# Performance work log

Hardware: AMD Instinct MI355X
Metric: run time of the kernel (lower is better)

Reference implementation:

```python
import jax, jax.numpy as jnp
import numpy as np

V, D, B, NEG = 100000, 128, 4096, 5
D_INNER = int(D * 2.0 * 2 / 3)  # nGPT FF inner dim = 170

def l2norm(t, axis=-1):
    return t / jnp.linalg.norm(t, axis=axis, keepdims=True)

def setup_inputs() -> dict:
    key = jax.random.key(0)
    ks = jax.random.split(key, 8)
    return {
        "input_ids": jax.random.randint(ks[0], (B,), 0, V),
        "target_ids": jax.random.randint(ks[1], (B,), 0, V),
        "neg_ids": jax.random.randint(ks[2], (B, NEG), 0, V),
        "W_in": jax.random.normal(ks[3], (V, D), jnp.float32) * (1.0 / np.sqrt(D)),
        "W_out": jax.random.normal(ks[4], (V, D), jnp.float32) * (1.0 / np.sqrt(D)),
        "W_hidden": jax.random.normal(ks[5], (D_INNER, D), jnp.float32) * 0.02,
        "W_gate": jax.random.normal(ks[6], (D_INNER, D), jnp.float32) * 0.02,
        "W_ff_out": jax.random.normal(ks[7], (D, D_INNER), jnp.float32) * 0.02,
        "hidden_scale": jnp.ones((D_INNER,), jnp.float32),
        "gate_scale": jnp.ones((D_INNER,), jnp.float32),
        "logit_scale": jnp.full((V,), D ** -0.5, dtype=jnp.float32),  # Scale param init = s_logit_scale
    }

def reference(input_ids, target_ids, neg_ids, W_in, W_out, W_hidden, W_gate,
              W_ff_out, hidden_scale, gate_scale, logit_scale):
    # skipgram: gather normalized input embeddings
    emb = l2norm(W_in)[input_ids]                                  # (B, D)
    # nGPT FeedForward: silu-gated, weights l2-normalized on input dim
    h = (emb @ l2norm(W_hidden).T) * hidden_scale                  # (B, D_INNER)
    g = (emb @ l2norm(W_gate).T) * gate_scale * jnp.sqrt(jnp.float32(D))
    x = jax.nn.silu(g) * h
    x = x @ l2norm(W_ff_out, axis=0).T                             # (B, D), to_out norm_dim_in=False
    # logits over full vocab, scaled by Scale(): param * (init/scale)
    scale_eff = logit_scale * (1.0 / (D ** -0.5))                  # (V,)
    logits = (x @ l2norm(W_out).T) * scale_eff                     # (B, V)
    # negative-sampling loss: gather positive + sampled negative logits
    pos = jnp.take_along_axis(logits, target_ids[:, None], axis=1)  # (B, 1)
    neg = jnp.take_along_axis(logits, neg_ids, axis=1)              # (B, NEG)
    positive_loss = jax.nn.log_sigmoid(pos).mean()
    negative_loss = jax.nn.log_sigmoid(-neg).mean()
    return -(positive_loss + negative_loss)
```

## Files before the change

kernel.cpp:

```cpp
#include <hip/hip_runtime.h>
#include <math.h>

#define DD    128
#define DI    170
#define DIP   176
#define ND4   32
#define ND4H  16
#define NI4P  44
#define BB    4096
#define NNEG  5
#define ROWS  8
#define NBLK  (BB / ROWS)
#define NTHR  512
#define NTASK (ROWS * (1 + NNEG))
#define XOP   132
#define SQRT_D 11.3137084989847603904f

#define WS_WHT 0
#define WS_WGT (ND4 * DIP * 4)
#define WS_WFT (2 * ND4 * DIP * 4)

__device__ __forceinline__ float wave_bcast_sum(float v) {
#pragma unroll
    for (int m = 1; m < 64; m <<= 1) v += __shfl_xor(v, m, 64);
    return v;
}

__global__ __launch_bounds__(256) void prep_kernel(
    const float* __restrict__ W_hidden,
    const float* __restrict__ W_gate,
    const float* __restrict__ W_ff_out,
    const float* __restrict__ hidden_scale,
    const float* __restrict__ gate_scale,
    float* __restrict__ ws,
    float* __restrict__ out)
{
    if (blockIdx.x == 0 && threadIdx.x == 0) out[0] = 0.0f;
    const int wave = threadIdx.x >> 6;
    const int lane = threadIdx.x & 63;
    const int t = blockIdx.x * 4 + wave;
    float* whT = ws + WS_WHT;
    float* wgT = ws + WS_WGT;
    float* wfT = ws + WS_WFT;

    if (t < DI) {
        const int v = t;
        float a = W_ff_out[(long)(2 * lane)     * DI + v];
        float b = W_ff_out[(long)(2 * lane + 1) * DI + v];
        float cf = wave_bcast_sum(a * a + b * b);
        float2 ph = ((const float2*)(W_hidden + (long)v * DD))[lane];
        float2 pg = ((const float2*)(W_gate   + (long)v * DD))[lane];
        float sh = wave_bcast_sum(ph.x * ph.x + ph.y * ph.y);
        float sg = wave_bcast_sum(pg.x * pg.x + pg.y * pg.y);
        const float whs = rsqrtf(sh) * hidden_scale[v] * rsqrtf(cf);
        const float wgs = rsqrtf(sg) * gate_scale[v] * SQRT_D;
        const int d4   = lane >> 1;
        const int half = lane & 1;
        float2* dh = (float2*)(whT + ((long)d4 * DIP + v) * 4 + half * 2);
        *dh = make_float2(ph.x * whs, ph.y * whs);
        float2* dg = (float2*)(wgT + ((long)d4 * DIP + v) * 4 + half * 2);
        *dg = make_float2(pg.x * wgs, pg.y * wgs);
    } else if (t < DI + NI4P) {
        const int i4 = t - DI;
#pragma unroll
        for (int rr = 0; rr < 2; ++rr) {
            const int dd = rr * 64 + lane;
            float4 v4;
            if (i4 < 42) {
                float2 lo = *(const float2*)(W_ff_out + (long)dd * DI + 4 * i4);
                float2 hi = *(const float2*)(W_ff_out + (long)dd * DI + 4 * i4 + 2);
                v4 = make_float4(lo.x, lo.y, hi.x, hi.y);
            } else if (i4 == 42) {
                float2 lo = *(const float2*)(W_ff_out + (long)dd * DI + 168);
                v4 = make_float4(lo.x, lo.y, 0.0f, 0.0f);
            } else {
                v4 = make_float4(0.0f, 0.0f, 0.0f, 0.0f);
            }
            *(float4*)(wfT + ((long)i4 * DD + dd) * 4) = v4;
        }
    } else if (t == DI + NI4P || t == DI + NI4P + 1) {
        float* base = (t == DI + NI4P) ? whT : wgT;
        for (int idx = lane; idx < ND4 * 6; idx += 64) {
            const int d4 = idx / 6, c = idx % 6;
            *(float4*)(base + ((long)d4 * DIP + DI + c) * 4) =
                make_float4(0.0f, 0.0f, 0.0f, 0.0f);
        }
    }
}

__global__ __launch_bounds__(NTHR, 4) void main_kernel(
    const int*   __restrict__ input_ids,
    const int*   __restrict__ target_ids,
    const int*   __restrict__ neg_ids,
    const float* __restrict__ W_in,
    const float* __restrict__ W_out,
    const float* __restrict__ logit_scale,
    const float* __restrict__ ws,
    float* __restrict__ out)
{
    __shared__ __align__(16) float s_emb[ROWS][DD];
    __shared__ __align__(16) float s_x[ROWS][DIP];
    __shared__ __align__(16) float s_pp[8][ROWS][DD];
    __shared__ __align__(16) float s_xout[ROWS][XOP];
    __shared__ float s_part[DIP][2 * ROWS + 1];
    __shared__ float s_dp[NTASK][9];
    __shared__ float s_sp[NTASK][9];
    __shared__ float s_psc[NTASK];
    __shared__ float s_ls[NTASK];

    const int tid  = threadIdx.x;
    const int wave = tid >> 6;
    const int lane = tid & 63;
    const int b0   = blockIdx.x * ROWS;

    const float4* whT4 = (const float4*)(ws + WS_WHT);
    const float4* wgT4 = (const float4*)(ws + WS_WGT);
    const float4* wfT4 = (const float4*)(ws + WS_WFT);

    {
        const int id = input_ids[b0 + wave];
        float2 p = ((const float2*)(W_in + (long)id * DD))[lane];
        float s  = wave_bcast_sum(p.x * p.x + p.y * p.y);
        float inv = rsqrtf(s);
        s_emb[wave][2 * lane]     = p.x * inv;
        s_emb[wave][2 * lane + 1] = p.y * inv;
    }
    __syncthreads();

    const bool gA = (tid < DIP);
    const bool gB = (tid >= 256 && tid < 256 + DIP);
    const int i = gA ? tid : (gB ? tid - 256 : -1);
    float ah[ROWS], ag[ROWS];
#pragma unroll
    for (int r = 0; r < ROWS; ++r) { ah[r] = 0.0f; ag[r] = 0.0f; }

    if (i >= 0) {
        const int d4lo = gA ? 0 : ND4H;
#pragma unroll 4
        for (int k = 0; k < ND4H; ++k) {
            const int d4 = d4lo + k;
            float4 h4 = whT4[d4 * DIP + i];
            float4 g4 = wgT4[d4 * DIP + i];
#pragma unroll
            for (int r = 0; r < ROWS; ++r) {
                float4 e4 = ((const float4*)s_emb[r])[d4];
                ah[r] += e4.x * h4.x + e4.y * h4.y + e4.z * h4.z + e4.w * h4.w;
                ag[r] += e4.x * g4.x + e4.y * g4.y + e4.z * g4.z + e4.w * g4.w;
            }
        }
    }
    if (gB) {
#pragma unroll
        for (int r = 0; r < ROWS; ++r) {
            s_part[i][r]        = ah[r];
            s_part[i][ROWS + r] = ag[r];
        }
    }
    __syncthreads();

    if (gA) {
#pragma unroll
        for (int r = 0; r < ROWS; ++r) {
            float h = ah[r] + s_part[i][r];
            float g = ag[r] + s_part[i][ROWS + r];
            float x = (g / (1.0f + __expf(-g))) * h;
            s_x[r][i] = x;
        }
    }
    __syncthreads();

    {
        const int i4lo = (wave < 4) ? 6 * wave : 24 + 5 * (wave - 4);
        const int i4n  = (wave < 4) ? 6 : 5;
        float acc0[ROWS], acc1[ROWS];
#pragma unroll
        for (int r = 0; r < ROWS; ++r) { acc0[r] = 0.0f; acc1[r] = 0.0f; }
        for (int k = 0; k < i4n; ++k) {
            const int i4 = i4lo + k;
            float4 wa = wfT4[i4 * DD + lane];
            float4 wb = wfT4[i4 * DD + 64 + lane];
#pragma unroll
            for (int r = 0; r < ROWS; ++r) {
                float4 x4 = ((const float4*)s_x[r])[i4];
                acc0[r] += wa.x * x4.x + wa.y * x4.y + wa.z * x4.z + wa.w * x4.w;
                acc1[r] += wb.x * x4.x + wb.y * x4.y + wb.z * x4.z + wb.w * x4.w;
            }
        }
#pragma unroll
        for (int r = 0; r < ROWS; ++r) {
            s_pp[wave][r][lane]      = acc0[r];
            s_pp[wave][r][64 + lane] = acc1[r];
        }
    }
    __syncthreads();

    {
        const int dd = tid & 127;
        const int r0 = tid >> 7;
#pragma unroll
        for (int rr = 0; rr < 2; ++rr) {
            const int r = r0 + 4 * rr;
            float v = s_pp[0][r][dd];
#pragma unroll
            for (int q = 1; q < 8; ++q) v += s_pp[q][r][dd];
            s_xout[r][dd] = v;
        }
    }
    __syncthreads();

    if (tid < NTASK * 8) {
        const int t  = tid >> 3;
        const int c  = tid & 7;
        const int r  = t / (1 + NNEG);
        const int jj = t % (1 + NNEG);
        const int bidx = b0 + r;
        const int id = (jj == 0) ? target_ids[bidx] : neg_ids[bidx * NNEG + jj - 1];
        if (c == 0) s_psc[t] = logit_scale[id];
        const float4* wrow4 = (const float4*)(W_out + (long)id * DD);
        const float4* xr4   = (const float4*)&s_xout[r][0];
        float dot = 0.0f, ss = 0.0f;
#pragma unroll
        for (int k2 = 0; k2 < 4; ++k2) {
            const int j = c + 8 * k2;
            float4 w4 = wrow4[j];
            float4 x4 = xr4[j];
            dot += w4.x * x4.x + w4.y * x4.y + w4.z * x4.z + w4.w * x4.w;
            ss  += w4.x * w4.x + w4.y * w4.y + w4.z * w4.z + w4.w * w4.w;
        }
        s_dp[t][c] = dot;
        s_sp[t][c] = ss;
    }
    __syncthreads();

    if (tid < NTASK) {
        const int t  = tid;
        const int jj = t % (1 + NNEG);
        float dot = s_dp[t][0], ss = s_sp[t][0];
#pragma unroll
        for (int c = 1; c < 8; ++c) { dot += s_dp[t][c]; ss += s_sp[t][c]; }
        const float logit = dot * rsqrtf(ss) * s_psc[t] * SQRT_D;
        const float z  = (jj == 0) ? logit : -logit;
        const float ls = fminf(z, 0.0f) - log1pf(__expf(-fabsf(z)));
        s_ls[t] = (jj == 0) ? ls * (1.0f / BB) : ls * (1.0f / (BB * NNEG));
    }
    __syncthreads();
    if (tid == 0) {
        float tot = 0.0f;
#pragma unroll
        for (int t = 0; t < NTASK; ++t) tot += s_ls[t];
        atomicAdd(out, -tot);
    }
}

extern "C" void kernel_launch(void* const* d_in, const int* in_sizes, int n_in,
                              void* d_out, int out_size, void* d_ws, size_t ws_size,
                              hipStream_t stream) {
    (void)in_sizes; (void)n_in; (void)out_size; (void)ws_size;
    const int*   input_ids    = (const int*)  d_in[0];
    const int*   target_ids   = (const int*)  d_in[1];
    const int*   neg_ids      = (const int*)  d_in[2];
    const float* W_in         = (const float*)d_in[3];
    const float* W_out        = (const float*)d_in[4];
    const float* W_hidden     = (const float*)d_in[5];
    const float* W_gate       = (const float*)d_in[6];
    const float* W_ff_out     = (const float*)d_in[7];
    const float* hidden_scale = (const float*)d_in[8];
    const float* gate_scale   = (const float*)d_in[9];
    const float* logit_scale  = (const float*)d_in[10];
    float* out = (float*)d_out;
    float* ws  = (float*)d_ws;

    prep_kernel<<<54, 256, 0, stream>>>(W_hidden, W_gate, W_ff_out,
                                        hidden_scale, gate_scale, ws, out);
    main_kernel<<<NBLK, NTHR, 0, stream>>>(input_ids, target_ids, neg_ids,
                                           W_in, W_out, logit_scale, ws, out);
}
```

Before: 148.5 us.

## Prefetch gathered W_out rows into LDS via async loads during the feed-forward phase

Waves 3 and 7 sit idle during the hidden/gate projection. They now look up the target and negative ids, then issue global_load_lds copies of the matching W_out rows and their logit_scale values into a new shared buffer. The later logit dot products read those rows from LDS, so the random-gather latency overlaps with the feed-forward compute instead of following it. The output projection is also reorganised so each thread covers one output column over 11 float4 chunks, cutting the partial sums to be reduced from 8 to 4 and shrinking s_pp. Plain __syncthreads are replaced with an lgkmcnt-only barrier. That barrier does not explicitly wait on vmcnt, which tracks the async LDS DMA loads, so correctness relies on the compiler inserting that wait. LDS use per block also grows.

```diff
diff --git a/kernel.cpp b/kernel.cpp
--- a/kernel.cpp
+++ b/kernel.cpp
@@ -19,6 +19,13 @@
 #define WS_WHT 0
 #define WS_WGT (ND4 * DIP * 4)
 #define WS_WFT (2 * ND4 * DIP * 4)
+
+#define GLOAD_LDS4(gptr, lptr)                                                  \
+    __builtin_amdgcn_global_load_lds(                                           \
+        (const __attribute__((address_space(1))) void*)(gptr),                  \
+        (__attribute__((address_space(3))) void*)(lptr), 4, 0, 0)
+
+#define BAR_LGKM() asm volatile("s_waitcnt lgkmcnt(0)\n\ts_barrier" ::: "memory")
 
 __device__ __forceinline__ float wave_bcast_sum(float v) {
 #pragma unroll
@@ -100,8 +107,9 @@
 {
     __shared__ __align__(16) float s_emb[ROWS][DD];
     __shared__ __align__(16) float s_x[ROWS][DIP];
-    __shared__ __align__(16) float s_pp[8][ROWS][DD];
+    __shared__ __align__(16) float s_pp[4][ROWS][DD];
     __shared__ __align__(16) float s_xout[ROWS][XOP];
+    __shared__ __align__(16) float s_wout[NTASK][DD];
     __shared__ float s_part[DIP][2 * ROWS + 1];
     __shared__ float s_dp[NTASK][9];
     __shared__ float s_sp[NTASK][9];
@@ -125,7 +133,7 @@
         s_emb[wave][2 * lane]     = p.x * inv;
         s_emb[wave][2 * lane + 1] = p.y * inv;
     }
-    __syncthreads();
+    BAR_LGKM();
 
     const bool gA = (tid < DIP);
     const bool gB = (tid >= 256 && tid < 256 + DIP);
@@ -148,6 +156,27 @@
                 ag[r] += e4.x * g4.x + e4.y * g4.y + e4.z * g4.z + e4.w * g4.w;
             }
         }
+    } else if (wave == 3 || wave == 7) {
+        const int tb = (wave == 3) ? 0 : 24;
+        int   myid  = 0;
+        float mypsc = 0.0f;
+        if (lane < 24) {
+            const int t  = tb + lane;
+            const int r  = t / (1 + NNEG);
+            const int jj = t % (1 + NNEG);
+            const int bidx = b0 + r;
+            myid  = (jj == 0) ? target_ids[bidx] : neg_ids[bidx * NNEG + jj - 1];
+            mypsc = logit_scale[myid];
+        }
+#pragma unroll
+        for (int k = 0; k < 24; ++k) {
+            const int t   = tb + k;
+            const int idt = __shfl(myid, k, 64);
+            const float* gsrc = W_out + (long)idt * DD;
+            GLOAD_LDS4(gsrc + lane,      &s_wout[t][0]);
+            GLOAD_LDS4(gsrc + 64 + lane, &s_wout[t][64]);
+        }
+        if (lane < 24) s_psc[tb + lane] = mypsc;
     }
     if (gB) {
 #pragma unroll
@@ -156,7 +185,7 @@
             s_part[i][ROWS + r] = ag[r];
         }
     }
-    __syncthreads();
+    BAR_LGKM();
 
     if (gA) {
 #pragma unroll
@@ -167,32 +196,29 @@
             s_x[r][i] = x;
         }
     }
-    __syncthreads();
+    BAR_LGKM();
 
     {
-        const int i4lo = (wave < 4) ? 6 * wave : 24 + 5 * (wave - 4);
-        const int i4n  = (wave < 4) ? 6 : 5;
-        float acc0[ROWS], acc1[ROWS];
-#pragma unroll
-        for (int r = 0; r < ROWS; ++r) { acc0[r] = 0.0f; acc1[r] = 0.0f; }
-        for (int k = 0; k < i4n; ++k) {
+        const int dd = tid & 127;
+        const int q  = tid >> 7;
+        const int i4lo = q * 11;
+        float acc[ROWS];
+#pragma unroll
+        for (int r = 0; r < ROWS; ++r) acc[r] = 0.0f;
+#pragma unroll 4
+        for (int k = 0; k < 11; ++k) {
             const int i4 = i4lo + k;
-            float4 wa = wfT4[i4 * DD + lane];
-            float4 wb = wfT4[i4 * DD + 64 + lane];
+            float4 w4 = wfT4[i4 * DD + dd];
 #pragma unroll
             for (int r = 0; r < ROWS; ++r) {
                 float4 x4 = ((const float4*)s_x[r])[i4];
-                acc0[r] += wa.x * x4.x + wa.y * x4.y + wa.z * x4.z + wa.w * x4.w;
-                acc1[r] += wb.x * x4.x + wb.y * x4.y + wb.z * x4.z + wb.w * x4.w;
+                acc[r] += w4.x * x4.x + w4.y * x4.y + w4.z * x4.z + w4.w * x4.w;
             }
         }
 #pragma unroll
-        for (int r = 0; r < ROWS; ++r) {
-            s_pp[wave][r][lane]      = acc0[r];
-            s_pp[wave][r][64 + lane] = acc1[r];
-        }
-    }
-    __syncthreads();
+        for (int r = 0; r < ROWS; ++r) s_pp[q][r][dd] = acc[r];
+    }
+    BAR_LGKM();
 
     {
         const int dd = tid & 127;
@@ -200,9 +226,8 @@
 #pragma unroll
         for (int rr = 0; rr < 2; ++rr) {
             const int r = r0 + 4 * rr;
-            float v = s_pp[0][r][dd];
-#pragma unroll
-            for (int q = 1; q < 8; ++q) v += s_pp[q][r][dd];
+            float v = ((s_pp[0][r][dd] + s_pp[1][r][dd])
+                       + s_pp[2][r][dd]) + s_pp[3][r][dd];
             s_xout[r][dd] = v;
         }
     }
@@ -212,11 +237,7 @@
         const int t  = tid >> 3;
         const int c  = tid & 7;
         const int r  = t / (1 + NNEG);
-        const int jj = t % (1 + NNEG);
-        const int bidx = b0 + r;
-        const int id = (jj == 0) ? target_ids[bidx] : neg_ids[bidx * NNEG + jj - 1];
-        if (c == 0) s_psc[t] = logit_scale[id];
-        const float4* wrow4 = (const float4*)(W_out + (long)id * DD);
+        const float4* wrow4 = (const float4*)&s_wout[t][0];
         const float4* xr4   = (const float4*)&s_xout[r][0];
         float dot = 0.0f, ss = 0.0f;
 #pragma unroll
```

New measurement: 148.9 us, median of 2. Within noise of the previous version (+0.3%).
